# Kernel tuning notes

Hardware: AMD Instinct MI355X
Metric: run time of the kernel (lower is better)

Reference implementation:

```python
import jax, jax.numpy as jnp
import numpy as np

N_NODES = 50000
N_EDGES = 800000
D_FEAT = 64


def setup_inputs() -> dict:
    key = jax.random.key(0)
    kx, ks, kd = jax.random.split(key, 3)
    x = jax.random.normal(kx, (N_NODES, D_FEAT), dtype=jnp.float32)
    src = jax.random.randint(ks, (N_EDGES,), 0, N_NODES, dtype=jnp.int64)
    dst = jax.random.randint(kd, (N_EDGES,), 0, N_NODES, dtype=jnp.int64)
    return {"x": x, "src": src, "dst": dst}


def reference(x, src, dst):
    # SGC propagation: h[v] = sum_{(u->v) in E} x[u] / sqrt(out_deg(u) * out_deg(v))
    n = x.shape[0]
    # out-degrees: count of outgoing edges per node (matches graph.out_degrees())
    deg = jax.ops.segment_sum(jnp.ones(src.shape, x.dtype), src, num_segments=n)
    # per-edge normalization coefficient 1/sqrt(deg_u * deg_v)  [E]
    norm = 1.0 / jnp.sqrt(deg[src] * deg[dst])
    # gather-multiply-scatter-sum (u_mul_e_sum): messages flow src -> dst
    h = jax.ops.segment_sum(x[src] * norm[:, None], dst, num_segments=n)
    return h
```

## Files before the change

### kernel.cpp

```cpp
#include <hip/hip_runtime.h>

#define N_NODES 50000
#define N_EDGES 800000
#define D_FEAT 64

#define NBINS 1024
#define BSORT 100
#define SORT_CHUNK (N_EDGES / BSORT)
#define NSCAN (NBINS * BSORT)
#define SCAN_BLOCK 1024
#define SCAN_BLOCKS (NSCAN / SCAN_BLOCK)
#define AGG_CAP 3072
#define NAGG ((N_NODES + 63) / 64)

#define HCHUNKS 64
#define HCHUNK (N_EDGES / HCHUNKS)
#define HWORDS ((N_NODES + 3) / 4)

#define RS_BLOCKS ((N_NODES + 255) / 256)

__global__ __launch_bounds__(512)
void hist_count_kernel(const int* __restrict__ src, const int* __restrict__ dst,
                       unsigned int* __restrict__ hp32, unsigned int* __restrict__ gh) {
    __shared__ unsigned int lh[HWORDS];
    const int b = blockIdx.x, t = threadIdx.x;
    if (b < HCHUNKS) {
        for (int i = t; i < HWORDS; i += 512) lh[i] = 0u;
        __syncthreads();
        const int4* s4 = (const int4*)(src + b * HCHUNK);
        for (int i = t; i < HCHUNK / 4; i += 512) {
            int4 v = s4[i];
            atomicAdd(&lh[v.x >> 2], 1u << ((v.x & 3) * 8));
            atomicAdd(&lh[v.y >> 2], 1u << ((v.y & 3) * 8));
            atomicAdd(&lh[v.z >> 2], 1u << ((v.z & 3) * 8));
            atomicAdd(&lh[v.w >> 2], 1u << ((v.w & 3) * 8));
        }
        __syncthreads();
        for (int w = t; w < HWORDS; w += 512)
            hp32[(size_t)b * HWORDS + w] = lh[w];
    } else {
        const int cb = b - HCHUNKS;
        for (int i = t; i < NBINS; i += 512) lh[i] = 0;
        __syncthreads();
        const int4* d4 = (const int4*)(dst + cb * SORT_CHUNK);
        for (int i = t; i < SORT_CHUNK / 4; i += 512) {
            int4 v = d4[i];
            atomicAdd(&lh[v.x >> 6], 1u);
            atomicAdd(&lh[v.y >> 6], 1u);
            atomicAdd(&lh[v.z >> 6], 1u);
            atomicAdd(&lh[v.w >> 6], 1u);
        }
        __syncthreads();
        for (int i = t; i < NBINS; i += 512) gh[(size_t)i * BSORT + cb] = lh[i];
    }
}

__global__ __launch_bounds__(SCAN_BLOCK)
void scanred_rs_kernel(const unsigned int* __restrict__ gh, unsigned int* __restrict__ partial,
                       const unsigned char* __restrict__ hp8, float* __restrict__ rs) {
    const int b = blockIdx.x;
    if (b < SCAN_BLOCKS) {
        __shared__ unsigned int wsum[SCAN_BLOCK / 64];
        int g = b * SCAN_BLOCK + threadIdx.x;
        unsigned int v = gh[g];
        for (int off = 32; off > 0; off >>= 1) v += __shfl_down(v, off, 64);
        if ((threadIdx.x & 63) == 0) wsum[threadIdx.x >> 6] = v;
        __syncthreads();
        if (threadIdx.x < SCAN_BLOCK / 64) {
            unsigned int s = wsum[threadIdx.x];
            for (int off = SCAN_BLOCK / 128; off > 0; off >>= 1) s += __shfl_down(s, off, 64);
            if (threadIdx.x == 0) partial[b] = s;
        }
    } else {
        if (threadIdx.x < 256) {
            int v = (b - SCAN_BLOCKS) * 256 + threadIdx.x;
            if (v < N_NODES) {
                unsigned int s = 0;
                #pragma unroll
                for (int c = 0; c < HCHUNKS; ++c) s += hp8[(size_t)c * (HWORDS * 4) + v];
                rs[v] = rsqrtf((float)s);
            }
        }
    }
}

__global__ __launch_bounds__(SCAN_BLOCK)
void scan_final_kernel(unsigned int* __restrict__ data, const unsigned int* __restrict__ partial) {
    __shared__ unsigned int wsum[SCAN_BLOCK / 64];
    __shared__ unsigned int red2[2];
    const int t = threadIdx.x;
    const int lane = t & 63;
    const int wid = t >> 6;
    const int g = blockIdx.x * SCAN_BLOCK + t;

    unsigned int p = (t < blockIdx.x) ? partial[t] : 0u;
    if (t < 128) {
        for (int off = 32; off > 0; off >>= 1) p += __shfl_down(p, off, 64);
        if (lane == 0) red2[wid] = p;
    }

    unsigned int v = data[g];
    unsigned int sc = v;
    for (int off = 1; off < 64; off <<= 1) {
        unsigned int u = __shfl_up(sc, off, 64);
        if (lane >= off) sc += u;
    }
    if (lane == 63) wsum[wid] = sc;
    __syncthreads();
    if (t < SCAN_BLOCK / 64) {
        unsigned int q = wsum[t];
        for (int off = 1; off < SCAN_BLOCK / 64; off <<= 1) {
            unsigned int u = __shfl_up(q, off, 64);
            if (t >= off) q += u;
        }
        wsum[t] = q;
    }
    __syncthreads();
    const unsigned int base = red2[0] + red2[1];
    const unsigned int wbase = (wid == 0) ? 0u : wsum[wid - 1];
    data[g] = base + wbase + sc - v;
}

__global__ __launch_bounds__(1024)
void bucket_scatter_kernel(const int* __restrict__ src, const int* __restrict__ dst,
                           const unsigned int* __restrict__ gh, unsigned int* __restrict__ keysB) {
    __shared__ unsigned int cur[NBINS];
    const int b = blockIdx.x, t = threadIdx.x;
    if (t < NBINS) cur[t] = gh[(size_t)t * BSORT + b];
    __syncthreads();
    const int4* s4 = (const int4*)(src + b * SORT_CHUNK);
    const int4* d4 = (const int4*)(dst + b * SORT_CHUNK);
    for (int i = t; i < SORT_CHUNK / 4; i += 1024) {
        int4 s = s4[i];
        int4 d = d4[i];
        unsigned int p0 = atomicAdd(&cur[d.x >> 6], 1u);
        keysB[p0] = ((unsigned int)d.x << 16) | (unsigned int)s.x;
        unsigned int p1 = atomicAdd(&cur[d.y >> 6], 1u);
        keysB[p1] = ((unsigned int)d.y << 16) | (unsigned int)s.y;
        unsigned int p2 = atomicAdd(&cur[d.z >> 6], 1u);
        keysB[p2] = ((unsigned int)d.z << 16) | (unsigned int)s.z;
        unsigned int p3 = atomicAdd(&cur[d.w >> 6], 1u);
        keysB[p3] = ((unsigned int)d.w << 16) | (unsigned int)s.w;
    }
}

__global__ __launch_bounds__(512)
void bucket_aggregate_kernel(const float* __restrict__ x, const unsigned int* __restrict__ gh,
                             const unsigned int* __restrict__ keysB, const float* __restrict__ rs,
                             float* __restrict__ h) {
    __shared__ unsigned int ebuf[AGG_CAP];
    __shared__ unsigned int ecnt[64];
    __shared__ unsigned int eoff[65];
    const int g = blockIdx.x;
    const int t = threadIdx.x;
    const int lane = t & 63;
    const int w = t >> 6;
    const unsigned int base = gh[(size_t)g * BSORT];
    const unsigned int end  = gh[(size_t)(g + 1) * BSORT];
    const int cnt = (int)(end - base);

    if (cnt > 0 && cnt <= AGG_CAP) {
        if (t < 64) ecnt[t] = 0;
        __syncthreads();
        for (int i = t; i < cnt; i += 512) atomicAdd(&ecnt[(keysB[base + i] >> 16) & 63], 1u);
        __syncthreads();
        if (t < 64) {
            unsigned int c = ecnt[t];
            unsigned int q = c;
            for (int off = 1; off < 64; off <<= 1) {
                unsigned int u = __shfl_up(q, off, 64);
                if (lane >= off) q += u;
            }
            eoff[t] = q - c;
            if (t == 63) eoff[64] = q;
        }
        __syncthreads();
        if (t < 64) ecnt[t] = eoff[t];
        __syncthreads();
        for (int i = t; i < cnt; i += 512) {
            unsigned int k = keysB[base + i];
            ebuf[atomicAdd(&ecnt[(k >> 16) & 63], 1u)] = k;
        }
        __syncthreads();

        const int grp = lane >> 4;
        const int fl  = lane & 15;
        for (int nl = w; nl < 64; nl += 8) {
            int node = g * 64 + nl;
            if (node >= N_NODES) continue;
            const int jb = (int)eoff[nl];
            const int m  = (int)eoff[nl + 1] - jb;
            float ax = 0.0f, ay = 0.0f, az = 0.0f, aw = 0.0f;
            int jj = 0;
            for (; jj + 8 <= m; jj += 8) {
                unsigned int s0 = ebuf[jb + jj + grp] & 0xFFFFu;
                unsigned int s1 = ebuf[jb + jj + 4 + grp] & 0xFFFFu;
                const float4 v0 = *(const float4*)&x[(size_t)s0 * D_FEAT + fl * 4];
                const float4 v1 = *(const float4*)&x[(size_t)s1 * D_FEAT + fl * 4];
                float w0 = rs[s0], w1 = rs[s1];
                ax = fmaf(v0.x, w0, ax); ay = fmaf(v0.y, w0, ay);
                az = fmaf(v0.z, w0, az); aw = fmaf(v0.w, w0, aw);
                ax = fmaf(v1.x, w1, ax); ay = fmaf(v1.y, w1, ay);
                az = fmaf(v1.z, w1, az); aw = fmaf(v1.w, w1, aw);
            }
            if (jj < m) {
                int idx = jj + grp;
                unsigned int s = ebuf[jb + min(idx, m - 1)] & 0xFFFFu;
                float wgt = (idx < m) ? rs[s] : 0.0f;
                const float4 v = *(const float4*)&x[(size_t)s * D_FEAT + fl * 4];
                ax = fmaf(v.x, wgt, ax); ay = fmaf(v.y, wgt, ay);
                az = fmaf(v.z, wgt, az); aw = fmaf(v.w, wgt, aw);
                jj += 4;
                if (jj < m) {
                    idx = jj + grp;
                    unsigned int s2 = ebuf[jb + min(idx, m - 1)] & 0xFFFFu;
                    float wgt2 = (idx < m) ? rs[s2] : 0.0f;
                    const float4 v2 = *(const float4*)&x[(size_t)s2 * D_FEAT + fl * 4];
                    ax = fmaf(v2.x, wgt2, ax); ay = fmaf(v2.y, wgt2, ay);
                    az = fmaf(v2.z, wgt2, az); aw = fmaf(v2.w, wgt2, aw);
                }
            }
            ax += __shfl_xor(ax, 16, 64); ay += __shfl_xor(ay, 16, 64);
            az += __shfl_xor(az, 16, 64); aw += __shfl_xor(aw, 16, 64);
            ax += __shfl_xor(ax, 32, 64); ay += __shfl_xor(ay, 32, 64);
            az += __shfl_xor(az, 32, 64); aw += __shfl_xor(aw, 32, 64);
            if (lane < 16) {
                float4 o;
                if (m > 0) {
                    const float rsn = rs[node];
                    o.x = ax * rsn; o.y = ay * rsn; o.z = az * rsn; o.w = aw * rsn;
                } else {
                    o.x = o.y = o.z = o.w = 0.0f;
                }
                *(float4*)&h[(size_t)node * D_FEAT + fl * 4] = o;
            }
        }
    } else {
        for (int nl = w; nl < 64; nl += 8) {
            int node = g * 64 + nl;
            if (node >= N_NODES) continue;
            float acc = 0.0f;
            int any = 0;
            for (unsigned int j = base; j < end; ++j) {
                unsigned int k = keysB[j];
                if ((int)((k >> 16) & 63) == nl) {
                    unsigned int s = k & 0xFFFFu;
                    acc = fmaf(x[(size_t)s * D_FEAT + lane], rs[s], acc);
                    any = 1;
                }
            }
            h[(size_t)node * D_FEAT + lane] = any ? acc * rs[node] : 0.0f;
        }
    }
}

__global__ void fb_degree_kernel(const int* __restrict__ src, unsigned int* __restrict__ deg,
                                 int n_edges) {
    int i = blockIdx.x * blockDim.x + threadIdx.x;
    int stride = gridDim.x * blockDim.x;
    for (; i < n_edges; i += stride) atomicAdd(&deg[src[i]], 1u);
}
__global__ void fb_scatter_kernel(const float* __restrict__ x, const int* __restrict__ src,
                                  const int* __restrict__ dst, const unsigned int* __restrict__ deg,
                                  float* __restrict__ h, int n_edges) {
    const int lane = threadIdx.x & 63;
    const int wave = (int)((blockIdx.x * blockDim.x + threadIdx.x) >> 6);
    const int nwaves = (int)((gridDim.x * blockDim.x) >> 6);
    for (int e = wave; e < n_edges; e += nwaves) {
        int s = __builtin_amdgcn_readfirstlane(src[e]);
        int d = __builtin_amdgcn_readfirstlane(dst[e]);
        float norm = rsqrtf((float)deg[s] * (float)deg[d]);
        atomicAdd(&h[d * D_FEAT + lane], x[s * D_FEAT + lane] * norm);
    }
}

extern "C" void kernel_launch(void* const* d_in, const int* in_sizes, int n_in,
                              void* d_out, int out_size, void* d_ws, size_t ws_size,
                              hipStream_t stream) {
    const float* x   = (const float*)d_in[0];
    const int*   src = (const int*)d_in[1];
    const int*   dst = (const int*)d_in[2];
    float* h = (float*)d_out;

    size_t off = 0;
    unsigned int*  keysB = (unsigned int*)((char*)d_ws + off);  off += (size_t)N_EDGES * 4;
    unsigned int*  hp32  = keysB;
    unsigned int*  gh    = (unsigned int*)((char*)d_ws + off);  off += (size_t)NSCAN * 4;
    float*         rs    = (float*)((char*)d_ws + off);         off += (size_t)N_NODES * 4;
    unsigned int*  spart = (unsigned int*)((char*)d_ws + off);  off += 128 * 4;

    if (ws_size >= off) {
        hist_count_kernel<<<dim3(HCHUNKS + BSORT), dim3(512), 0, stream>>>(src, dst, hp32, gh);
        scanred_rs_kernel<<<dim3(SCAN_BLOCKS + RS_BLOCKS), dim3(SCAN_BLOCK), 0, stream>>>(
            gh, spart, (const unsigned char*)hp32, rs);
        scan_final_kernel<<<dim3(SCAN_BLOCKS), dim3(SCAN_BLOCK), 0, stream>>>(gh, spart);
        bucket_scatter_kernel<<<dim3(BSORT), dim3(1024), 0, stream>>>(src, dst, gh, keysB);
        bucket_aggregate_kernel<<<dim3(NAGG), dim3(512), 0, stream>>>(x, gh, keysB, rs, h);
    } else {
        unsigned int* deg = (unsigned int*)d_ws;
        hipMemsetAsync(deg, 0, N_NODES * sizeof(unsigned int), stream);
        hipMemsetAsync(d_out, 0, (size_t)out_size * sizeof(float), stream);
        fb_degree_kernel<<<dim3(1024), dim3(256), 0, stream>>>(src, deg, N_EDGES);
        fb_scatter_kernel<<<dim3(2048), dim3(256), 0, stream>>>(x, src, dst, deg, h, N_EDGES);
    }
}
```

Before: 57.78 us.

## Replace two-pass global scan with per-bin row scan and in-scatter bin offset scan

Removes the separate scan_final kernel. A per-bin wave now scans the BSORT chunk counts within each bin row and emits bin totals, and the scatter kernel scans the 1024 bin totals itself to get global bin offsets. The aggregate kernel reads these bin offsets, so there is one fewer launch and the multi-block scan is gone. BSORT is doubled to 200 so the scatter and histogram stages get more blocks, at the cost of a redundant 1024-element scan in every scatter block and a bigger per-chunk histogram table.

```diff
diff --git a/kernel.cpp b/kernel.cpp
--- a/kernel.cpp
+++ b/kernel.cpp
@@ -5,11 +5,9 @@
 #define D_FEAT 64
 
 #define NBINS 1024
-#define BSORT 100
+#define BSORT 200
 #define SORT_CHUNK (N_EDGES / BSORT)
 #define NSCAN (NBINS * BSORT)
-#define SCAN_BLOCK 1024
-#define SCAN_BLOCKS (NSCAN / SCAN_BLOCK)
 #define AGG_CAP 3072
 #define NAGG ((N_NODES + 63) / 64)
 
@@ -17,7 +15,8 @@
 #define HCHUNK (N_EDGES / HCHUNKS)
 #define HWORDS ((N_NODES + 3) / 4)
 
-#define RS_BLOCKS ((N_NODES + 255) / 256)
+#define BINSCAN_BLOCKS (NBINS / 16)
+#define RS_BLOCKS ((N_NODES + 1023) / 1024)
 
 __global__ __launch_bounds__(512)
 void hist_count_kernel(const int* __restrict__ src, const int* __restrict__ dst,
@@ -55,79 +54,77 @@
     }
 }
 
-__global__ __launch_bounds__(SCAN_BLOCK)
-void scanred_rs_kernel(const unsigned int* __restrict__ gh, unsigned int* __restrict__ partial,
+__global__ __launch_bounds__(1024)
+void binscan_rs_kernel(unsigned int* __restrict__ gh, unsigned int* __restrict__ binsum,
                        const unsigned char* __restrict__ hp8, float* __restrict__ rs) {
-    const int b = blockIdx.x;
-    if (b < SCAN_BLOCKS) {
-        __shared__ unsigned int wsum[SCAN_BLOCK / 64];
-        int g = b * SCAN_BLOCK + threadIdx.x;
-        unsigned int v = gh[g];
-        for (int off = 32; off > 0; off >>= 1) v += __shfl_down(v, off, 64);
-        if ((threadIdx.x & 63) == 0) wsum[threadIdx.x >> 6] = v;
-        __syncthreads();
-        if (threadIdx.x < SCAN_BLOCK / 64) {
-            unsigned int s = wsum[threadIdx.x];
-            for (int off = SCAN_BLOCK / 128; off > 0; off >>= 1) s += __shfl_down(s, off, 64);
-            if (threadIdx.x == 0) partial[b] = s;
-        }
+    const int b = blockIdx.x, t = threadIdx.x;
+    if (b < BINSCAN_BLOCKS) {
+        const int lane = t & 63;
+        const int i = b * 16 + (t >> 6);
+        uint4 c = make_uint4(0u, 0u, 0u, 0u);
+        unsigned int* row = gh + (size_t)i * BSORT;
+        if (lane * 4 < BSORT) c = *(const uint4*)(row + lane * 4);
+        unsigned int tot = c.x + c.y + c.z + c.w;
+        unsigned int q = tot;
+        for (int off = 1; off < 64; off <<= 1) {
+            unsigned int u = __shfl_up(q, off, 64);
+            if (lane >= off) q += u;
+        }
+        const unsigned int ebase = q - tot;
+        if (lane * 4 < BSORT) {
+            uint4 o;
+            o.x = ebase;
+            o.y = ebase + c.x;
+            o.z = ebase + c.x + c.y;
+            o.w = ebase + c.x + c.y + c.z;
+            *(uint4*)(row + lane * 4) = o;
+        }
+        unsigned int total = __shfl(q, 63, 64);
+        if (lane == 0) binsum[i] = total;
     } else {
-        if (threadIdx.x < 256) {
-            int v = (b - SCAN_BLOCKS) * 256 + threadIdx.x;
-            if (v < N_NODES) {
-                unsigned int s = 0;
-                #pragma unroll
-                for (int c = 0; c < HCHUNKS; ++c) s += hp8[(size_t)c * (HWORDS * 4) + v];
-                rs[v] = rsqrtf((float)s);
-            }
-        }
-    }
-}
-
-__global__ __launch_bounds__(SCAN_BLOCK)
-void scan_final_kernel(unsigned int* __restrict__ data, const unsigned int* __restrict__ partial) {
-    __shared__ unsigned int wsum[SCAN_BLOCK / 64];
-    __shared__ unsigned int red2[2];
-    const int t = threadIdx.x;
-    const int lane = t & 63;
-    const int wid = t >> 6;
-    const int g = blockIdx.x * SCAN_BLOCK + t;
-
-    unsigned int p = (t < blockIdx.x) ? partial[t] : 0u;
-    if (t < 128) {
-        for (int off = 32; off > 0; off >>= 1) p += __shfl_down(p, off, 64);
-        if (lane == 0) red2[wid] = p;
-    }
-
-    unsigned int v = data[g];
-    unsigned int sc = v;
-    for (int off = 1; off < 64; off <<= 1) {
-        unsigned int u = __shfl_up(sc, off, 64);
-        if (lane >= off) sc += u;
-    }
-    if (lane == 63) wsum[wid] = sc;
-    __syncthreads();
-    if (t < SCAN_BLOCK / 64) {
-        unsigned int q = wsum[t];
-        for (int off = 1; off < SCAN_BLOCK / 64; off <<= 1) {
-            unsigned int u = __shfl_up(q, off, 64);
-            if (t >= off) q += u;
-        }
-        wsum[t] = q;
-    }
-    __syncthreads();
-    const unsigned int base = red2[0] + red2[1];
-    const unsigned int wbase = (wid == 0) ? 0u : wsum[wid - 1];
-    data[g] = base + wbase + sc - v;
+        int v = (b - BINSCAN_BLOCKS) * 1024 + t;
+        if (v < N_NODES) {
+            unsigned int s = 0;
+            #pragma unroll
+            for (int c2 = 0; c2 < HCHUNKS; ++c2) s += hp8[(size_t)c2 * (HWORDS * 4) + v];
+            rs[v] = rsqrtf((float)s);
+        }
+    }
 }
 
 __global__ __launch_bounds__(1024)
 void bucket_scatter_kernel(const int* __restrict__ src, const int* __restrict__ dst,
-                           const unsigned int* __restrict__ gh, unsigned int* __restrict__ keysB) {
+                           const unsigned int* __restrict__ gh,
+                           const unsigned int* __restrict__ binsum,
+                           unsigned int* __restrict__ binoffG,
+                           unsigned int* __restrict__ keysB) {
     __shared__ unsigned int cur[NBINS];
+    __shared__ unsigned int wsums[16];
     const int b = blockIdx.x, t = threadIdx.x;
-    if (t < NBINS) cur[t] = gh[(size_t)t * BSORT + b];
+    const int lane = t & 63, wid = t >> 6;
+
+    unsigned int bs = binsum[t];
+    unsigned int q = bs;
+    for (int off = 1; off < 64; off <<= 1) {
+        unsigned int u = __shfl_up(q, off, 64);
+        if (lane >= off) q += u;
+    }
+    if (lane == 63) wsums[wid] = q;
     __syncthreads();
+    if (t < 16) {
+        unsigned int r = wsums[t];
+        for (int off = 1; off < 16; off <<= 1) {
+            unsigned int u = __shfl_up(r, off, 64);
+            if (t >= off) r += u;
+        }
+        wsums[t] = r;
+    }
+    __syncthreads();
+    const unsigned int binoff = ((wid ? wsums[wid - 1] : 0u) + q) - bs;
+    cur[t] = binoff + gh[(size_t)t * BSORT + b];
+    if (b == 0) binoffG[t] = binoff;
+    __syncthreads();
+
     const int4* s4 = (const int4*)(src + b * SORT_CHUNK);
     const int4* d4 = (const int4*)(dst + b * SORT_CHUNK);
     for (int i = t; i < SORT_CHUNK / 4; i += 1024) {
@@ -145,7 +142,8 @@
 }
 
 __global__ __launch_bounds__(512)
-void bucket_aggregate_kernel(const float* __restrict__ x, const unsigned int* __restrict__ gh,
+void bucket_aggregate_kernel(const float* __restrict__ x,
+                             const unsigned int* __restrict__ binoffG,
                              const unsigned int* __restrict__ keysB, const float* __restrict__ rs,
                              float* __restrict__ h) {
     __shared__ unsigned int ebuf[AGG_CAP];
@@ -155,8 +153,8 @@
     const int t = threadIdx.x;
     const int lane = t & 63;
     const int w = t >> 6;
-    const unsigned int base = gh[(size_t)g * BSORT];
-    const unsigned int end  = gh[(size_t)(g + 1) * BSORT];
+    const unsigned int base = binoffG[g];
+    const unsigned int end  = (g + 1 < NBINS) ? binoffG[g + 1] : (unsigned int)N_EDGES;
     const int cnt = (int)(end - base);
 
     if (cnt > 0 && cnt <= AGG_CAP) {
@@ -283,19 +281,20 @@
     float* h = (float*)d_out;
 
     size_t off = 0;
-    unsigned int*  keysB = (unsigned int*)((char*)d_ws + off);  off += (size_t)N_EDGES * 4;
-    unsigned int*  hp32  = keysB;
-    unsigned int*  gh    = (unsigned int*)((char*)d_ws + off);  off += (size_t)NSCAN * 4;
-    float*         rs    = (float*)((char*)d_ws + off);         off += (size_t)N_NODES * 4;
-    unsigned int*  spart = (unsigned int*)((char*)d_ws + off);  off += 128 * 4;
+    unsigned int*  keysB   = (unsigned int*)((char*)d_ws + off);  off += (size_t)N_EDGES * 4;
+    unsigned int*  hp32    = keysB;
+    unsigned int*  gh      = (unsigned int*)((char*)d_ws + off);  off += (size_t)NSCAN * 4;
+    float*         rs      = (float*)((char*)d_ws + off);         off += (size_t)N_NODES * 4;
+    unsigned int*  binsum  = (unsigned int*)((char*)d_ws + off);  off += NBINS * 4;
+    unsigned int*  binoffG = (unsigned int*)((char*)d_ws + off);  off += NBINS * 4;
 
     if (ws_size >= off) {
         hist_count_kernel<<<dim3(HCHUNKS + BSORT), dim3(512), 0, stream>>>(src, dst, hp32, gh);
-        scanred_rs_kernel<<<dim3(SCAN_BLOCKS + RS_BLOCKS), dim3(SCAN_BLOCK), 0, stream>>>(
-            gh, spart, (const unsigned char*)hp32, rs);
-        scan_final_kernel<<<dim3(SCAN_BLOCKS), dim3(SCAN_BLOCK), 0, stream>>>(gh, spart);
-        bucket_scatter_kernel<<<dim3(BSORT), dim3(1024), 0, stream>>>(src, dst, gh, keysB);
-        bucket_aggregate_kernel<<<dim3(NAGG), dim3(512), 0, stream>>>(x, gh, keysB, rs, h);
+        binscan_rs_kernel<<<dim3(BINSCAN_BLOCKS + RS_BLOCKS), dim3(1024), 0, stream>>>(
+            gh, binsum, (const unsigned char*)hp32, rs);
+        bucket_scatter_kernel<<<dim3(BSORT), dim3(1024), 0, stream>>>(src, dst, gh, binsum,
+                                                                      binoffG, keysB);
+        bucket_aggregate_kernel<<<dim3(NAGG), dim3(512), 0, stream>>>(x, binoffG, keysB, rs, h);
     } else {
         unsigned int* deg = (unsigned int*)d_ws;
         hipMemsetAsync(deg, 0, N_NODES * sizeof(unsigned int), stream);
```

Measured after the change: 56.14 us. -2.8%, faster.
